# Kernel tuning notes

Measured on AMD Instinct MI355X. Metric: run time of the kernel, lower is better.

Reference implementation:

```python
import jax, jax.numpy as jnp
import numpy as np

B, N, V, H, Z = 2048, 32, 10, 256, 64


def setup_inputs() -> dict:
    key = jax.random.key(0)
    ks = jax.random.split(key, 14)
    # strictly upper-triangular random DAG adjacency (topological order = vertex index)
    p = jax.random.uniform(ks[0], (B, N, N))
    tri = jnp.triu(jnp.ones((N, N), jnp.float32), k=1)
    adj = (p < 0.12).astype(jnp.float32) * tri
    node_types = jax.random.randint(ks[1], (B, N), 0, V).astype(jnp.int32)
    s = 0.05
    return dict(
        adj=adj,
        node_types=node_types,
        w_ih=jax.random.normal(ks[2], (V, 3 * H), jnp.float32) * s,
        w_hh=jax.random.normal(ks[3], (H, 3 * H), jnp.float32) * s,
        b_ih=jax.random.normal(ks[4], (3 * H,), jnp.float32) * s,
        b_hh=jax.random.normal(ks[5], (3 * H,), jnp.float32) * s,
        w_gate=jax.random.normal(ks[6], (H, H), jnp.float32) * s,
        b_gate=jax.random.normal(ks[7], (H,), jnp.float32) * s,
        w_map=jax.random.normal(ks[8], (H, H), jnp.float32) * s,
        w_mu=jax.random.normal(ks[9], (H, Z), jnp.float32) * s,
        b_mu=jax.random.normal(ks[10], (Z,), jnp.float32) * s,
        w_std=jax.random.normal(ks[11], (H, Z), jnp.float32) * s,
        b_std=jax.random.normal(ks[12], (Z,), jnp.float32) * s,
    )


def _gru_cell(x, h, w_ih, w_hh, b_ih, b_hh):
    # torch GRUCell math; weights stored [in, 3H]
    gi = x @ w_ih + b_ih  # [B, 3H]
    gh = h @ w_hh + b_hh
    i_r, i_z, i_n = jnp.split(gi, 3, axis=-1)
    h_r, h_z, h_n = jnp.split(gh, 3, axis=-1)
    r = jax.nn.sigmoid(i_r + h_r)
    z = jax.nn.sigmoid(i_z + h_z)
    n = jnp.tanh(i_n + r * h_n)
    return (1.0 - z) * n + z * h


def reference(adj, node_types, w_ih, w_hh, b_ih, b_hh, w_gate, b_gate, w_map,
              w_mu, b_mu, w_std, b_std):
    x_all = jax.nn.one_hot(node_types, V, dtype=adj.dtype)  # [B, N, V]
    hidden0 = jnp.zeros((B, N, H), adj.dtype)
    adj_cols = jnp.transpose(adj, (2, 0, 1))  # [N, B, N]; col v = predecessor mask of v
    x_seq = jnp.transpose(x_all, (1, 0, 2))   # [N, B, V]

    def step(hidden, inps):
        col, x, v = inps
        # gate(h_pred) * map(h_pred), summed over predecessors. map has no bias,
        # so non-predecessor (zero-masked) rows contribute exactly zero, matching
        # the padded-gather formulation in the original code.
        gm = jax.nn.sigmoid(hidden @ w_gate + b_gate) * (hidden @ w_map)  # [B, N, H]
        agg = jnp.einsum('bn,bnh->bh', col, gm)  # [B, H]; zero for v=0 (no preds)
        h_new = _gru_cell(x, agg, w_ih, w_hh, b_ih, b_hh)  # [B, H]
        hidden = jax.lax.dynamic_update_slice(hidden, h_new[:, None, :], (0, v, 0))
        return hidden, None

    hidden, _ = jax.lax.scan(step, hidden0, (adj_cols, x_seq, jnp.arange(N)))
    hg = hidden[:, -1, :]  # graph state = last vertex hidden
    mu = hg @ w_mu + b_mu
    sigma = hg @ w_std + b_std
    return (mu, sigma)
```

## Files before the change

### kernel.cpp

```cpp
#include <hip/hip_runtime.h>


#define BB 2048
#define NN 32
#define VV 10
#define HH 256
#define ZZ 64
#define BT 8
#define KC 8
#define NT1 48
#define NT2 32
#define WHH_ELEMS (NT1 * KC * 64 * 8)
#define WGM_ELEMS (NT2 * KC * 64 * 8)
#define DYN_LDS_BYTES (BT * NN * HH * 2)

typedef __attribute__((ext_vector_type(8))) short frag8;
typedef __attribute__((ext_vector_type(4))) float facc4;

__device__ __forceinline__ float bf2f(unsigned short u) {
    unsigned int x = ((unsigned int)u) << 16;
    return __builtin_bit_cast(float, x);
}
__device__ __forceinline__ unsigned short f2bf(float f) {
    unsigned int x = __builtin_bit_cast(unsigned int, f);
    x += 0x7FFFu + ((x >> 16) & 1u);
    return (unsigned short)(x >> 16);
}
__device__ __forceinline__ float sigm(float x) { return 1.0f / (1.0f + __expf(-x)); }
__device__ __forceinline__ float ldv(const float* p, size_t i) { return p[i]; }
__device__ __forceinline__ float ldv(const unsigned short* p, size_t i) { return bf2f(p[i]); }
__device__ __forceinline__ void stv(float* p, size_t i, float v) { p[i] = v; }
__device__ __forceinline__ void stv(unsigned short* p, size_t i, float v) { p[i] = f2bf(v); }

__global__ void detect_dtype(const unsigned short* __restrict__ w, int* flag) {
    __shared__ int zc, bc;
    if (threadIdx.x == 0) { zc = 0; bc = 0; }
    __syncthreads();
    int z = 0, b = 0;
    for (int i = threadIdx.x; i < 2048; i += 256) {
        unsigned short lo = w[2 * i];
        if (lo == 0) z++;
        unsigned e = (lo >> 7) & 0xFFu;
        if (e >= 0x86u) b++;
    }
    atomicAdd(&zc, z); atomicAdd(&bc, b);
    __syncthreads();
    if (threadIdx.x == 0) *flag = (bc > 0 || zc > 512) ? 1 : 0;
}

template <typename T>
__global__ void repack_weights(const T* __restrict__ w_hh,
                               const T* __restrict__ w_gate,
                               const T* __restrict__ w_map,
                               unsigned short* __restrict__ whh_p,
                               unsigned short* __restrict__ wgm_p,
                               const int* __restrict__ flag, int want) {
    if (*flag != want) return;
    int t = blockIdx.x * blockDim.x + threadIdx.x;
    int lane = t & 63;
    int frag = t >> 6;
    int kbase = (lane >> 4) * 8;
    if (frag < NT1 * KC) {
        int jt = frag / KC, kc = frag % KC;
        int col = jt * 16 + (lane & 15);
        unsigned short* dst = whh_p + ((size_t)frag * 64 + lane) * 8;
        #pragma unroll
        for (int j = 0; j < 8; ++j)
            dst[j] = f2bf(ldv(w_hh, (size_t)(kc * 32 + kbase + j) * 768 + col));
    } else if (frag < (NT1 + NT2) * KC) {
        int f2 = frag - NT1 * KC;
        int jt = f2 / KC, kc = f2 % KC;
        int col = jt * 16 + (lane & 15);
        unsigned short* dst = wgm_p + ((size_t)f2 * 64 + lane) * 8;
        #pragma unroll
        for (int j = 0; j < 8; ++j) {
            int k = kc * 32 + kbase + j;
            dst[j] = f2bf((col < HH) ? ldv(w_gate, (size_t)k * HH + col)
                                     : ldv(w_map, (size_t)k * HH + (col - HH)));
        }
    }
}

template <typename T>
__global__ __launch_bounds__(1024, 4) void vae_main(
    const T* __restrict__ adj,
    const int* __restrict__ ntypes,
    const T* __restrict__ w_ih,
    const T* __restrict__ b_ih,
    const T* __restrict__ b_hh,
    const T* __restrict__ b_gate,
    const T* __restrict__ w_mu,
    const T* __restrict__ b_mu,
    const T* __restrict__ w_std,
    const T* __restrict__ b_std,
    const unsigned short* __restrict__ whh_p,
    const unsigned short* __restrict__ wgm_p,
    T* __restrict__ out,
    const int* __restrict__ flag, int want)
{
    if (*flag != want) return;

    extern __shared__ __align__(16) char dyn_lds[];
    unsigned short* gmS = (unsigned short*)dyn_lds;

    __shared__ __align__(16) float agg[BT][HH];
    __shared__ __align__(16) unsigned short aggbf[BT][264];
    __shared__ __align__(16) unsigned short hnew[BT][264];
    __shared__ unsigned int  amask[BT][NN];
    __shared__ int           ntva[BT][NN];
    __shared__ unsigned short bihL[768], bhhL[768], bgL[HH];

    const int tid  = threadIdx.x;
    const int lane = tid & 63;
    const int w    = tid >> 6;
    const int b0   = blockIdx.x * BT;

    const frag8* whh8 = (const frag8*)whh_p;
    const frag8* wgm8 = (const frag8*)wgm_p;

    if (tid < 256) {
        int bi = tid >> 5, vv = tid & 31;
        unsigned m = 0;
        for (int n = 0; n < NN; ++n)
            if (ldv(adj, ((size_t)(b0 + bi) * NN + n) * NN + vv) != 0.0f) m |= (1u << n);
        amask[bi][vv] = m;
    } else if (tid < 512) {
        int idx = tid - 256;
        int bi = idx >> 5, vv = idx & 31;
        ntva[bi][vv] = ntypes[(b0 + bi) * NN + vv];
    }
    for (int i = tid; i < 768; i += 1024) {
        bihL[i] = f2bf(ldv(b_ih, i));
        bhhL[i] = f2bf(ldv(b_hh, i));
    }
    if (tid < HH) bgL[tid] = f2bf(ldv(b_gate, tid));

    frag8 wR[KC], wG[KC];
    {
        const frag8* pR = whh8 + (size_t)w * (KC * 64) + lane;
        const frag8* pG = wgm8 + (size_t)w * (KC * 64) + lane;
        #pragma unroll
        for (int kc = 0; kc < KC; ++kc) { wR[kc] = pR[kc * 64]; wG[kc] = pG[kc * 64]; }
    }
    __syncthreads();

    const int arow  = lane & 15;
    const int acol0 = (lane >> 4) * 8;

    for (int v = 0; v < NN; ++v) {
        if (w < BT) {
            const int bi = w;
            const int h4 = lane * 4;
            const unsigned short* rb = gmS + (size_t)(bi * NN) * HH + h4;
            unsigned m = amask[bi][v];
            float a0 = 0.f, a1 = 0.f, a2 = 0.f, a3 = 0.f;
            float c0 = 0.f, c1 = 0.f, c2 = 0.f, c3 = 0.f;
            while (m) {
                int n0 = __builtin_ctz(m); m &= m - 1;
                const ushort4 g0 = *(const ushort4*)(rb + n0 * HH);
                if (m) {
                    int n1 = __builtin_ctz(m); m &= m - 1;
                    const ushort4 g1 = *(const ushort4*)(rb + n1 * HH);
                    c0 += bf2f(g1.x); c1 += bf2f(g1.y);
                    c2 += bf2f(g1.z); c3 += bf2f(g1.w);
                }
                a0 += bf2f(g0.x); a1 += bf2f(g0.y);
                a2 += bf2f(g0.z); a3 += bf2f(g0.w);
            }
            a0 += c0; a1 += c1; a2 += c2; a3 += c3;
            *(float4*)&agg[bi][h4] = make_float4(a0, a1, a2, a3);
            ushort4 ab; ab.x = f2bf(a0); ab.y = f2bf(a1); ab.z = f2bf(a2); ab.w = f2bf(a3);
            *(ushort4*)&aggbf[bi][h4] = ab;
        }
        __syncthreads();

        {
            frag8 afrag[KC];
            if (arow < BT) {
                #pragma unroll
                for (int kc = 0; kc < KC; ++kc)
                    afrag[kc] = *(const frag8*)&aggbf[arow][kc * 32 + acol0];
            } else {
                #pragma unroll
                for (int kc = 0; kc < KC; ++kc) afrag[kc] = frag8{};
            }

            const int t = w;
            facc4 aR = {0.f, 0.f, 0.f, 0.f};
            facc4 aZ = {0.f, 0.f, 0.f, 0.f};
            facc4 aN = {0.f, 0.f, 0.f, 0.f};
            const frag8* pZ = whh8 + (size_t)(t + 16) * (KC * 64) + lane;
            const frag8* pN = whh8 + (size_t)(t + 32) * (KC * 64) + lane;
            #pragma unroll
            for (int kc = 0; kc < KC; ++kc) {
                aR = __builtin_amdgcn_mfma_f32_16x16x32_bf16(afrag[kc], wR[kc], aR, 0, 0, 0);
                aZ = __builtin_amdgcn_mfma_f32_16x16x32_bf16(afrag[kc], pZ[kc * 64], aZ, 0, 0, 0);
                aN = __builtin_amdgcn_mfma_f32_16x16x32_bf16(afrag[kc], pN[kc * 64], aN, 0, 0, 0);
            }
            const int col = t * 16 + (lane & 15);
            const int q = lane >> 4;
            if (q < 2) {
                const float bir  = bf2f(bihL[col]),       bhr = bf2f(bhhL[col]);
                const float biz  = bf2f(bihL[col + 256]), bhz = bf2f(bhhL[col + 256]);
                const float bin_ = bf2f(bihL[col + 512]), bhn = bf2f(bhhL[col + 512]);
                #pragma unroll
                for (int i = 0; i < 4; ++i) {
                    const int bi = 4 * q + i;
                    const size_t ty = (size_t)ntva[bi][v] * 768;
                    const float xr = ldv(w_ih, ty + col);
                    const float xz = ldv(w_ih, ty + col + 256);
                    const float xn = ldv(w_ih, ty + col + 512);
                    const float r = sigm(xr + bir + aR[i] + bhr);
                    const float z = sigm(xz + biz + aZ[i] + bhz);
                    const float n = tanhf(xn + bin_ + r * (aN[i] + bhn));
                    const float h = (1.f - z) * n + z * agg[bi][col];
                    hnew[bi][col] = f2bf(h);
                }
            }
        }
        __syncthreads();

        {
            frag8 hfrag[KC];
            if (arow < BT) {
                #pragma unroll
                for (int kc = 0; kc < KC; ++kc)
                    hfrag[kc] = *(const frag8*)&hnew[arow][kc * 32 + acol0];
            } else {
                #pragma unroll
                for (int kc = 0; kc < KC; ++kc) hfrag[kc] = frag8{};
            }

            const int t = w;
            facc4 aG = {0.f, 0.f, 0.f, 0.f};
            facc4 aM = {0.f, 0.f, 0.f, 0.f};
            const frag8* pM = wgm8 + (size_t)(t + 16) * (KC * 64) + lane;
            #pragma unroll
            for (int kc = 0; kc < KC; ++kc) {
                aG = __builtin_amdgcn_mfma_f32_16x16x32_bf16(hfrag[kc], wG[kc], aG, 0, 0, 0);
                aM = __builtin_amdgcn_mfma_f32_16x16x32_bf16(hfrag[kc], pM[kc * 64], aM, 0, 0, 0);
            }
            const int col = t * 16 + (lane & 15);
            const int q = lane >> 4;
            if (q < 2) {
                const float bg = bf2f(bgL[col]);
                #pragma unroll
                for (int i = 0; i < 4; ++i) {
                    const int bi = 4 * q + i;
                    gmS[(size_t)(bi * NN + v) * HH + col] = f2bf(sigm(aG[i] + bg) * aM[i]);
                }
            }
        }
        __syncthreads();
    }

    {
        const int bi = w >> 1, half = w & 1, z = lane;
        float am = 0.f, as = 0.f;
        const int h0 = half * 128;
        #pragma unroll 4
        for (int h = h0; h < h0 + 128; ++h) {
            const float hv = bf2f(hnew[bi][h]);
            am += hv * ldv(w_mu, (size_t)h * ZZ + z);
            as += hv * ldv(w_std, (size_t)h * ZZ + z);
        }
        agg[bi][half * 64 + z]       = am;
        agg[bi][128 + half * 64 + z] = as;
    }
    __syncthreads();
    if (w < BT) {
        const int bi = w, z = lane;
        const float am = agg[bi][z] + agg[bi][64 + z] + ldv(b_mu, z);
        const float as = agg[bi][128 + z] + agg[bi][192 + z] + ldv(b_std, z);
        stv(out, (size_t)(b0 + bi) * ZZ + z, am);
        stv(out, (size_t)BB * ZZ + (size_t)(b0 + bi) * ZZ + z, as);
    }
}

extern "C" void kernel_launch(void* const* d_in, const int* in_sizes, int n_in,
                              void* d_out, int out_size, void* d_ws, size_t ws_size,
                              hipStream_t stream)
{
    unsigned short* whh_p = (unsigned short*)d_ws;
    unsigned short* wgm_p = whh_p + WHH_ELEMS;

    size_t flag_off = (ws_size >= 8) ? ((ws_size - 4) & ~(size_t)3) : 0;
    int* flag = (int*)((char*)d_ws + flag_off);

    (void)hipFuncSetAttribute(reinterpret_cast<const void*>(&vae_main<float>),
                              hipFuncAttributeMaxDynamicSharedMemorySize, DYN_LDS_BYTES);
    (void)hipFuncSetAttribute(reinterpret_cast<const void*>(&vae_main<unsigned short>),
                              hipFuncAttributeMaxDynamicSharedMemorySize, DYN_LDS_BYTES);

    detect_dtype<<<dim3(1), 256, 0, stream>>>((const unsigned short*)d_in[2], flag);

    repack_weights<float><<<dim3(160), 256, 0, stream>>>(
        (const float*)d_in[3], (const float*)d_in[6], (const float*)d_in[8],
        whh_p, wgm_p, flag, 1);
    repack_weights<unsigned short><<<dim3(160), 256, 0, stream>>>(
        (const unsigned short*)d_in[3], (const unsigned short*)d_in[6],
        (const unsigned short*)d_in[8], whh_p, wgm_p, flag, 0);

    vae_main<float><<<dim3(BB / BT), 1024, DYN_LDS_BYTES, stream>>>(
        (const float*)d_in[0], (const int*)d_in[1], (const float*)d_in[2],
        (const float*)d_in[4], (const float*)d_in[5], (const float*)d_in[7],
        (const float*)d_in[9], (const float*)d_in[10], (const float*)d_in[11],
        (const float*)d_in[12], whh_p, wgm_p, (float*)d_out, flag, 1);
    vae_main<unsigned short><<<dim3(BB / BT), 1024, DYN_LDS_BYTES, stream>>>(
        (const unsigned short*)d_in[0], (const int*)d_in[1],
        (const unsigned short*)d_in[2], (const unsigned short*)d_in[4],
        (const unsigned short*)d_in[5], (const unsigned short*)d_in[7],
        (const unsigned short*)d_in[9], (const unsigned short*)d_in[10],
        (const unsigned short*)d_in[11], (const unsigned short*)d_in[12],
        whh_p, wgm_p, (unsigned short*)d_out, flag, 0);
}
```

Baseline: 601.1 us.

## Halve workgroup to 512 threads with each wave computing two column tiles

Cuts the block from 16 to 8 waves, so each wave now handles two 16-column tiles of both the GRU and the gate/map matmuls. Weight fragments are reloaded from global memory each step instead of being kept in registers across the whole recurrence. Biases are kept in LDS as fp32, and the final mu/sigma projection is done by one wave per batch row, dropping a reduction and a barrier. This trades per-step weight reload traffic and lower thread-level parallelism for fewer waves contending at the barriers, and possibly more resident blocks per CU given LDS limits.

```diff
diff --git a/kernel.cpp b/kernel.cpp
--- a/kernel.cpp
+++ b/kernel.cpp
@@ -82,7 +82,7 @@
 }
 
 template <typename T>
-__global__ __launch_bounds__(1024, 4) void vae_main(
+__global__ __launch_bounds__(512, 2) void vae_main(
     const T* __restrict__ adj,
     const int* __restrict__ ntypes,
     const T* __restrict__ w_ih,
@@ -108,7 +108,7 @@
     __shared__ __align__(16) unsigned short hnew[BT][264];
     __shared__ unsigned int  amask[BT][NN];
     __shared__ int           ntva[BT][NN];
-    __shared__ unsigned short bihL[768], bhhL[768], bgL[HH];
+    __shared__ float bihL[768], bhhL[768], bgL[HH];
 
     const int tid  = threadIdx.x;
     const int lane = tid & 63;
@@ -124,31 +124,20 @@
         for (int n = 0; n < NN; ++n)
             if (ldv(adj, ((size_t)(b0 + bi) * NN + n) * NN + vv) != 0.0f) m |= (1u << n);
         amask[bi][vv] = m;
-    } else if (tid < 512) {
+    } else {
         int idx = tid - 256;
         int bi = idx >> 5, vv = idx & 31;
         ntva[bi][vv] = ntypes[(b0 + bi) * NN + vv];
     }
-    for (int i = tid; i < 768; i += 1024) {
-        bihL[i] = f2bf(ldv(b_ih, i));
-        bhhL[i] = f2bf(ldv(b_hh, i));
-    }
-    if (tid < HH) bgL[tid] = f2bf(ldv(b_gate, tid));
-
-    frag8 wR[KC], wG[KC];
-    {
-        const frag8* pR = whh8 + (size_t)w * (KC * 64) + lane;
-        const frag8* pG = wgm8 + (size_t)w * (KC * 64) + lane;
-        #pragma unroll
-        for (int kc = 0; kc < KC; ++kc) { wR[kc] = pR[kc * 64]; wG[kc] = pG[kc * 64]; }
-    }
+    for (int i = tid; i < 768; i += 512) { bihL[i] = ldv(b_ih, i); bhhL[i] = ldv(b_hh, i); }
+    if (tid < HH) bgL[tid] = ldv(b_gate, tid);
     __syncthreads();
 
     const int arow  = lane & 15;
     const int acol0 = (lane >> 4) * 8;
 
     for (int v = 0; v < NN; ++v) {
-        if (w < BT) {
+        {
             const int bi = w;
             const int h4 = lane * 4;
             const unsigned short* rb = gmS + (size_t)(bi * NN) * HH + h4;
@@ -185,36 +174,55 @@
                 for (int kc = 0; kc < KC; ++kc) afrag[kc] = frag8{};
             }
 
-            const int t = w;
-            facc4 aR = {0.f, 0.f, 0.f, 0.f};
-            facc4 aZ = {0.f, 0.f, 0.f, 0.f};
-            facc4 aN = {0.f, 0.f, 0.f, 0.f};
-            const frag8* pZ = whh8 + (size_t)(t + 16) * (KC * 64) + lane;
-            const frag8* pN = whh8 + (size_t)(t + 32) * (KC * 64) + lane;
+            frag8 R0[KC], Z0[KC], N0[KC], R1[KC], Z1[KC], N1[KC];
+            {
+                const frag8* pR0 = whh8 + (size_t)(w     ) * (KC * 64) + lane;
+                const frag8* pZ0 = whh8 + (size_t)(w + 16) * (KC * 64) + lane;
+                const frag8* pN0 = whh8 + (size_t)(w + 32) * (KC * 64) + lane;
+                const frag8* pR1 = whh8 + (size_t)(w +  8) * (KC * 64) + lane;
+                const frag8* pZ1 = whh8 + (size_t)(w + 24) * (KC * 64) + lane;
+                const frag8* pN1 = whh8 + (size_t)(w + 40) * (KC * 64) + lane;
+                #pragma unroll
+                for (int kc = 0; kc < KC; ++kc) {
+                    R0[kc] = pR0[kc * 64]; Z0[kc] = pZ0[kc * 64]; N0[kc] = pN0[kc * 64];
+                }
+                #pragma unroll
+                for (int kc = 0; kc < KC; ++kc) {
+                    R1[kc] = pR1[kc * 64]; Z1[kc] = pZ1[kc * 64]; N1[kc] = pN1[kc * 64];
+                }
+            }
+
             #pragma unroll
-            for (int kc = 0; kc < KC; ++kc) {
-                aR = __builtin_amdgcn_mfma_f32_16x16x32_bf16(afrag[kc], wR[kc], aR, 0, 0, 0);
-                aZ = __builtin_amdgcn_mfma_f32_16x16x32_bf16(afrag[kc], pZ[kc * 64], aZ, 0, 0, 0);
-                aN = __builtin_amdgcn_mfma_f32_16x16x32_bf16(afrag[kc], pN[kc * 64], aN, 0, 0, 0);
-            }
-            const int col = t * 16 + (lane & 15);
-            const int q = lane >> 4;
-            if (q < 2) {
-                const float bir  = bf2f(bihL[col]),       bhr = bf2f(bhhL[col]);
-                const float biz  = bf2f(bihL[col + 256]), bhz = bf2f(bhhL[col + 256]);
-                const float bin_ = bf2f(bihL[col + 512]), bhn = bf2f(bhhL[col + 512]);
-                #pragma unroll
-                for (int i = 0; i < 4; ++i) {
-                    const int bi = 4 * q + i;
-                    const size_t ty = (size_t)ntva[bi][v] * 768;
-                    const float xr = ldv(w_ih, ty + col);
-                    const float xz = ldv(w_ih, ty + col + 256);
-                    const float xn = ldv(w_ih, ty + col + 512);
-                    const float r = sigm(xr + bir + aR[i] + bhr);
-                    const float z = sigm(xz + biz + aZ[i] + bhz);
-                    const float n = tanhf(xn + bin_ + r * (aN[i] + bhn));
-                    const float h = (1.f - z) * n + z * agg[bi][col];
-                    hnew[bi][col] = f2bf(h);
+            for (int tt = 0; tt < 2; ++tt) {
+                const int t = w + tt * 8;
+                facc4 aR = {0.f, 0.f, 0.f, 0.f};
+                facc4 aZ = {0.f, 0.f, 0.f, 0.f};
+                facc4 aN = {0.f, 0.f, 0.f, 0.f};
+                #pragma unroll
+                for (int kc = 0; kc < KC; ++kc) {
+                    aR = __builtin_amdgcn_mfma_f32_16x16x32_bf16(afrag[kc], tt ? R1[kc] : R0[kc], aR, 0, 0, 0);
+                    aZ = __builtin_amdgcn_mfma_f32_16x16x32_bf16(afrag[kc], tt ? Z1[kc] : Z0[kc], aZ, 0, 0, 0);
+                    aN = __builtin_amdgcn_mfma_f32_16x16x32_bf16(afrag[kc], tt ? N1[kc] : N0[kc], aN, 0, 0, 0);
+                }
+                const int col = t * 16 + (lane & 15);
+                const int q = lane >> 4;
+                if (q < 2) {
+                    const float bir  = bihL[col],       bhr = bhhL[col];
+                    const float biz  = bihL[col + 256], bhz = bhhL[col + 256];
+                    const float bin_ = bihL[col + 512], bhn = bhhL[col + 512];
+                    #pragma unroll
+                    for (int i = 0; i < 4; ++i) {
+                        const int bi = 4 * q + i;
+                        const size_t ty = (size_t)ntva[bi][v] * 768;
+                        const float xr = ldv(w_ih, ty + col);
+                        const float xz = ldv(w_ih, ty + col + 256);
+                        const float xn = ldv(w_ih, ty + col + 512);
+                        const float r = sigm(xr + bir + aR[i] + bhr);
+                        const float z = sigm(xz + biz + aZ[i] + bhz);
+                        const float n = tanhf(xn + bin_ + r * (aN[i] + bhn));
+                        const float h = (1.f - z) * n + z * agg[bi][col];
+                        hnew[bi][col] = f2bf(h);
+                    }
                 }
             }
         }
@@ -231,23 +239,38 @@
                 for (int kc = 0; kc < KC; ++kc) hfrag[kc] = frag8{};
             }
 
-            const int t = w;
-            facc4 aG = {0.f, 0.f, 0.f, 0.f};
-            facc4 aM = {0.f, 0.f, 0.f, 0.f};
-            const frag8* pM = wgm8 + (size_t)(t + 16) * (KC * 64) + lane;
+            frag8 G0[KC], M0[KC], G1[KC], M1[KC];
+            {
+                const frag8* pG0 = wgm8 + (size_t)(w     ) * (KC * 64) + lane;
+                const frag8* pM0 = wgm8 + (size_t)(w + 16) * (KC * 64) + lane;
+                const frag8* pG1 = wgm8 + (size_t)(w +  8) * (KC * 64) + lane;
+                const frag8* pM1 = wgm8 + (size_t)(w + 24) * (KC * 64) + lane;
+                #pragma unroll
+                for (int kc = 0; kc < KC; ++kc) {
+                    G0[kc] = pG0[kc * 64]; M0[kc] = pM0[kc * 64];
+                    G1[kc] = pG1[kc * 64]; M1[kc] = pM1[kc * 64];
+                }
+            }
+
             #pragma unroll
-            for (int kc = 0; kc < KC; ++kc) {
-                aG = __builtin_amdgcn_mfma_f32_16x16x32_bf16(hfrag[kc], wG[kc], aG, 0, 0, 0);
-                aM = __builtin_amdgcn_mfma_f32_16x16x32_bf16(hfrag[kc], pM[kc * 64], aM, 0, 0, 0);
-            }
-            const int col = t * 16 + (lane & 15);
-            const int q = lane >> 4;
-            if (q < 2) {
-                const float bg = bf2f(bgL[col]);
-                #pragma unroll
-                for (int i = 0; i < 4; ++i) {
-                    const int bi = 4 * q + i;
-                    gmS[(size_t)(bi * NN + v) * HH + col] = f2bf(sigm(aG[i] + bg) * aM[i]);
+            for (int tt = 0; tt < 2; ++tt) {
+                const int t = w + tt * 8;
+                facc4 aG = {0.f, 0.f, 0.f, 0.f};
+                facc4 aM = {0.f, 0.f, 0.f, 0.f};
+                #pragma unroll
+                for (int kc = 0; kc < KC; ++kc) {
+                    aG = __builtin_amdgcn_mfma_f32_16x16x32_bf16(hfrag[kc], tt ? G1[kc] : G0[kc], aG, 0, 0, 0);
+                    aM = __builtin_amdgcn_mfma_f32_16x16x32_bf16(hfrag[kc], tt ? M1[kc] : M0[kc], aM, 0, 0, 0);
+                }
+                const int col = t * 16 + (lane & 15);
+                const int q = lane >> 4;
+                if (q < 2) {
+                    const float bg = bgL[col];
+                    #pragma unroll
+                    for (int i = 0; i < 4; ++i) {
+                        const int bi = 4 * q + i;
+                        gmS[(size_t)(bi * NN + v) * HH + col] = f2bf(sigm(aG[i] + bg) * aM[i]);
+                    }
                 }
             }
         }
@@ -255,23 +278,14 @@
     }
 
     {
-        const int bi = w >> 1, half = w & 1, z = lane;
-        float am = 0.f, as = 0.f;
-        const int h0 = half * 128;
-        #pragma unroll 4
-        for (int h = h0; h < h0 + 128; ++h) {
+        const int bi = w, z = lane;
+        float am = ldv(b_mu, z);
+        float as = ldv(b_std, z);
+        for (int h = 0; h < HH; ++h) {
             const float hv = bf2f(hnew[bi][h]);
             am += hv * ldv(w_mu, (size_t)h * ZZ + z);
             as += hv * ldv(w_std, (size_t)h * ZZ + z);
         }
-        agg[bi][half * 64 + z]       = am;
-        agg[bi][128 + half * 64 + z] = as;
-    }
-    __syncthreads();
-    if (w < BT) {
-        const int bi = w, z = lane;
-        const float am = agg[bi][z] + agg[bi][64 + z] + ldv(b_mu, z);
-        const float as = agg[bi][128 + z] + agg[bi][192 + z] + ldv(b_std, z);
         stv(out, (size_t)(b0 + bi) * ZZ + z, am);
         stv(out, (size_t)BB * ZZ + (size_t)(b0 + bi) * ZZ + z, as);
     }
@@ -301,12 +315,12 @@
         (const unsigned short*)d_in[3], (const unsigned short*)d_in[6],
         (const unsigned short*)d_in[8], whh_p, wgm_p, flag, 0);
 
-    vae_main<float><<<dim3(BB / BT), 1024, DYN_LDS_BYTES, stream>>>(
+    vae_main<float><<<dim3(BB / BT), 512, DYN_LDS_BYTES, stream>>>(
         (const float*)d_in[0], (const int*)d_in[1], (const float*)d_in[2],
         (const float*)d_in[4], (const float*)d_in[5], (const float*)d_in[7],
         (const float*)d_in[9], (const float*)d_in[10], (const float*)d_in[11],
         (const float*)d_in[12], whh_p, wgm_p, (float*)d_out, flag, 1);
-    vae_main<unsigned short><<<dim3(BB / BT), 1024, DYN_LDS_BYTES, stream>>>(
+    vae_main<unsigned short><<<dim3(BB / BT), 512, DYN_LDS_BYTES, stream>>>(
         (const unsigned short*)d_in[0], (const int*)d_in[1],
         (const unsigned short*)d_in[2], (const unsigned short*)d_in[4],
         (const unsigned short*)d_in[5], (const unsigned short*)d_in[7],
```

New measurement: 621.7 us. +3.4%, slower.

## Stage fused input weights in LDS, prefetch streamed MFMA weights, split aggregation across all waves

Applied to the files above, without the earlier changes.

The w_ih rows with b_ih folded in are staged into LDS as bf16, replacing per-step global loads of w_ih. The hidden-hidden and gate/map weight fragments are no longer held in registers; they are streamed from global memory with one-step-ahead software prefetch, which frees registers at the cost of more global or cache traffic. Predecessor aggregation now uses all 16 waves with 2 columns each, and the float agg buffer is dropped, so the GRU reads the previous hidden from the bf16 copy, which slightly lowers precision. The final mu/sigma projection is split by output instead of by half of H, removing one barrier.

```diff
diff --git a/kernel.cpp b/kernel.cpp
--- a/kernel.cpp
+++ b/kernel.cpp
@@ -103,12 +103,12 @@
     extern __shared__ __align__(16) char dyn_lds[];
     unsigned short* gmS = (unsigned short*)dyn_lds;
 
-    __shared__ __align__(16) float agg[BT][HH];
     __shared__ __align__(16) unsigned short aggbf[BT][264];
     __shared__ __align__(16) unsigned short hnew[BT][264];
+    __shared__ __align__(16) unsigned short wihL[VV * 776];
     __shared__ unsigned int  amask[BT][NN];
     __shared__ int           ntva[BT][NN];
-    __shared__ unsigned short bihL[768], bhhL[768], bgL[HH];
+    __shared__ float bhhL[768], bgL[HH];
 
     const int tid  = threadIdx.x;
     const int lane = tid & 63;
@@ -129,48 +129,37 @@
         int bi = idx >> 5, vv = idx & 31;
         ntva[bi][vv] = ntypes[(b0 + bi) * NN + vv];
     }
-    for (int i = tid; i < 768; i += 1024) {
-        bihL[i] = f2bf(ldv(b_ih, i));
-        bhhL[i] = f2bf(ldv(b_hh, i));
-    }
-    if (tid < HH) bgL[tid] = f2bf(ldv(b_gate, tid));
-
-    frag8 wR[KC], wG[KC];
-    {
-        const frag8* pR = whh8 + (size_t)w * (KC * 64) + lane;
-        const frag8* pG = wgm8 + (size_t)w * (KC * 64) + lane;
-        #pragma unroll
-        for (int kc = 0; kc < KC; ++kc) { wR[kc] = pR[kc * 64]; wG[kc] = pG[kc * 64]; }
-    }
+    for (int i = tid; i < VV * 768; i += 1024) {
+        int r = i / 768, c = i - r * 768;
+        wihL[r * 776 + c] = f2bf(ldv(w_ih, (size_t)i) + ldv(b_ih, (size_t)c));
+    }
+    for (int i = tid; i < 768; i += 1024) bhhL[i] = ldv(b_hh, i);
+    if (tid < HH) bgL[tid] = ldv(b_gate, tid);
     __syncthreads();
 
     const int arow  = lane & 15;
     const int acol0 = (lane >> 4) * 8;
 
     for (int v = 0; v < NN; ++v) {
-        if (w < BT) {
-            const int bi = w;
-            const int h4 = lane * 4;
-            const unsigned short* rb = gmS + (size_t)(bi * NN) * HH + h4;
+        {
+            const int bi = w >> 1;
+            const int c0 = (w & 1) * 128 + lane * 2;
+            const unsigned short* rb = gmS + (size_t)(bi * NN) * HH + c0;
             unsigned m = amask[bi][v];
-            float a0 = 0.f, a1 = 0.f, a2 = 0.f, a3 = 0.f;
-            float c0 = 0.f, c1 = 0.f, c2 = 0.f, c3 = 0.f;
+            float a0 = 0.f, a1 = 0.f, c0f = 0.f, c1f = 0.f;
             while (m) {
                 int n0 = __builtin_ctz(m); m &= m - 1;
-                const ushort4 g0 = *(const ushort4*)(rb + n0 * HH);
+                const ushort2 g0 = *(const ushort2*)(rb + n0 * HH);
                 if (m) {
                     int n1 = __builtin_ctz(m); m &= m - 1;
-                    const ushort4 g1 = *(const ushort4*)(rb + n1 * HH);
-                    c0 += bf2f(g1.x); c1 += bf2f(g1.y);
-                    c2 += bf2f(g1.z); c3 += bf2f(g1.w);
+                    const ushort2 g1 = *(const ushort2*)(rb + n1 * HH);
+                    c0f += bf2f(g1.x); c1f += bf2f(g1.y);
                 }
                 a0 += bf2f(g0.x); a1 += bf2f(g0.y);
-                a2 += bf2f(g0.z); a3 += bf2f(g0.w);
-            }
-            a0 += c0; a1 += c1; a2 += c2; a3 += c3;
-            *(float4*)&agg[bi][h4] = make_float4(a0, a1, a2, a3);
-            ushort4 ab; ab.x = f2bf(a0); ab.y = f2bf(a1); ab.z = f2bf(a2); ab.w = f2bf(a3);
-            *(ushort4*)&aggbf[bi][h4] = ab;
+            }
+            a0 += c0f; a1 += c1f;
+            ushort2 ab; ab.x = f2bf(a0); ab.y = f2bf(a1);
+            *(ushort2*)&aggbf[bi][c0] = ab;
         }
         __syncthreads();
 
@@ -186,35 +175,44 @@
             }
 
             const int t = w;
+            const frag8* pR = whh8 + (size_t)(t     ) * (KC * 64) + lane;
+            const frag8* pZ = whh8 + (size_t)(t + 16) * (KC * 64) + lane;
+            const frag8* pN = whh8 + (size_t)(t + 32) * (KC * 64) + lane;
+            frag8 bR = pR[0], bZ = pZ[0], bN = pN[0];
             facc4 aR = {0.f, 0.f, 0.f, 0.f};
             facc4 aZ = {0.f, 0.f, 0.f, 0.f};
             facc4 aN = {0.f, 0.f, 0.f, 0.f};
-            const frag8* pZ = whh8 + (size_t)(t + 16) * (KC * 64) + lane;
-            const frag8* pN = whh8 + (size_t)(t + 32) * (KC * 64) + lane;
             #pragma unroll
             for (int kc = 0; kc < KC; ++kc) {
-                aR = __builtin_amdgcn_mfma_f32_16x16x32_bf16(afrag[kc], wR[kc], aR, 0, 0, 0);
-                aZ = __builtin_amdgcn_mfma_f32_16x16x32_bf16(afrag[kc], pZ[kc * 64], aZ, 0, 0, 0);
-                aN = __builtin_amdgcn_mfma_f32_16x16x32_bf16(afrag[kc], pN[kc * 64], aN, 0, 0, 0);
+                frag8 nR{}, nZ{}, nN{};
+                if (kc + 1 < KC) {
+                    nR = pR[(kc + 1) * 64];
+                    nZ = pZ[(kc + 1) * 64];
+                    nN = pN[(kc + 1) * 64];
+                }
+                aR = __builtin_amdgcn_mfma_f32_16x16x32_bf16(afrag[kc], bR, aR, 0, 0, 0);
+                aZ = __builtin_amdgcn_mfma_f32_16x16x32_bf16(afrag[kc], bZ, aZ, 0, 0, 0);
+                aN = __builtin_amdgcn_mfma_f32_16x16x32_bf16(afrag[kc], bN, aN, 0, 0, 0);
+                bR = nR; bZ = nZ; bN = nN;
             }
             const int col = t * 16 + (lane & 15);
             const int q = lane >> 4;
             if (q < 2) {
-                const float bir  = bf2f(bihL[col]),       bhr = bf2f(bhhL[col]);
-                const float biz  = bf2f(bihL[col + 256]), bhz = bf2f(bhhL[col + 256]);
-                const float bin_ = bf2f(bihL[col + 512]), bhn = bf2f(bhhL[col + 512]);
+                const float bhr = bhhL[col];
+                const float bhz = bhhL[col + 256];
+                const float bhn = bhhL[col + 512];
                 #pragma unroll
                 for (int i = 0; i < 4; ++i) {
                     const int bi = 4 * q + i;
-                    const size_t ty = (size_t)ntva[bi][v] * 768;
-                    const float xr = ldv(w_ih, ty + col);
-                    const float xz = ldv(w_ih, ty + col + 256);
-                    const float xn = ldv(w_ih, ty + col + 512);
-                    const float r = sigm(xr + bir + aR[i] + bhr);
-                    const float z = sigm(xz + biz + aZ[i] + bhz);
-                    const float n = tanhf(xn + bin_ + r * (aN[i] + bhn));
-                    const float h = (1.f - z) * n + z * agg[bi][col];
-                    hnew[bi][col] = f2bf(h);
+                    const int ty = ntva[bi][v] * 776;
+                    const float xr = bf2f(wihL[ty + col]);
+                    const float xz = bf2f(wihL[ty + col + 256]);
+                    const float xn = bf2f(wihL[ty + col + 512]);
+                    const float r = sigm(xr + aR[i] + bhr);
+                    const float z = sigm(xz + aZ[i] + bhz);
+                    const float n = tanhf(xn + r * (aN[i] + bhn));
+                    const float hp = bf2f(aggbf[bi][col]);
+                    hnew[bi][col] = f2bf((1.f - z) * n + z * hp);
                 }
             }
         }
@@ -232,18 +230,26 @@
             }
 
             const int t = w;
+            const frag8* pG = wgm8 + (size_t)(t     ) * (KC * 64) + lane;
+            const frag8* pM = wgm8 + (size_t)(t + 16) * (KC * 64) + lane;
+            frag8 bG = pG[0], bM = pM[0];
             facc4 aG = {0.f, 0.f, 0.f, 0.f};
             facc4 aM = {0.f, 0.f, 0.f, 0.f};
-            const frag8* pM = wgm8 + (size_t)(t + 16) * (KC * 64) + lane;
             #pragma unroll
             for (int kc = 0; kc < KC; ++kc) {
-                aG = __builtin_amdgcn_mfma_f32_16x16x32_bf16(hfrag[kc], wG[kc], aG, 0, 0, 0);
-                aM = __builtin_amdgcn_mfma_f32_16x16x32_bf16(hfrag[kc], pM[kc * 64], aM, 0, 0, 0);
+                frag8 nG{}, nM{};
+                if (kc + 1 < KC) {
+                    nG = pG[(kc + 1) * 64];
+                    nM = pM[(kc + 1) * 64];
+                }
+                aG = __builtin_amdgcn_mfma_f32_16x16x32_bf16(hfrag[kc], bG, aG, 0, 0, 0);
+                aM = __builtin_amdgcn_mfma_f32_16x16x32_bf16(hfrag[kc], bM, aM, 0, 0, 0);
+                bG = nG; bM = nM;
             }
             const int col = t * 16 + (lane & 15);
             const int q = lane >> 4;
             if (q < 2) {
-                const float bg = bf2f(bgL[col]);
+                const float bg = bgL[col];
                 #pragma unroll
                 for (int i = 0; i < 4; ++i) {
                     const int bi = 4 * q + i;
@@ -255,25 +261,17 @@
     }
 
     {
-        const int bi = w >> 1, half = w & 1, z = lane;
-        float am = 0.f, as = 0.f;
-        const int h0 = half * 128;
+        const int bi = w & 7, z = lane;
+        const bool is_mu = (w < 8);
+        float acc = is_mu ? ldv(b_mu, z) : ldv(b_std, z);
+        const T* wm = is_mu ? w_mu : w_std;
         #pragma unroll 4
-        for (int h = h0; h < h0 + 128; ++h) {
+        for (int h = 0; h < HH; ++h) {
             const float hv = bf2f(hnew[bi][h]);
-            am += hv * ldv(w_mu, (size_t)h * ZZ + z);
-            as += hv * ldv(w_std, (size_t)h * ZZ + z);
-        }
-        agg[bi][half * 64 + z]       = am;
-        agg[bi][128 + half * 64 + z] = as;
-    }
-    __syncthreads();
-    if (w < BT) {
-        const int bi = w, z = lane;
-        const float am = agg[bi][z] + agg[bi][64 + z] + ldv(b_mu, z);
-        const float as = agg[bi][128 + z] + agg[bi][192 + z] + ldv(b_std, z);
-        stv(out, (size_t)(b0 + bi) * ZZ + z, am);
-        stv(out, (size_t)BB * ZZ + (size_t)(b0 + bi) * ZZ + z, as);
+            acc += hv * ldv(wm, (size_t)h * ZZ + z);
+        }
+        const size_t off = is_mu ? 0 : (size_t)BB * ZZ;
+        stv(out, off + (size_t)(b0 + bi) * ZZ + z, acc);
     }
 }
 
```

Result: no change. 603.4 us (+0.4%).

## Double batch tile to fill MFMA rows, spill half of gm state to global workspace

Applied to the files above, without the earlier changes.

Raises the per-block batch tile from 8 to 16 so every row of each 16x16 MFMA carries a real graph instead of zero padding, which halves the number of blocks. The gate*map state for the extra 8 graphs lives in a per-block global workspace slab because LDS only holds 8 graphs' worth. Weights are now streamed from global or cache in every step instead of being kept in registers, and the biases are stored in LDS as fp32. The main kernel is launched in chunks sized to the available workspace. The cost is extra global-memory traffic and latency on the serial 32-step recurrence.

```diff
diff --git a/kernel.cpp b/kernel.cpp
--- a/kernel.cpp
+++ b/kernel.cpp
@@ -6,13 +6,17 @@
 #define VV 10
 #define HH 256
 #define ZZ 64
-#define BT 8
+#define BT 16
 #define KC 8
 #define NT1 48
 #define NT2 32
 #define WHH_ELEMS (NT1 * KC * 64 * 8)
 #define WGM_ELEMS (NT2 * KC * 64 * 8)
-#define DYN_LDS_BYTES (BT * NN * HH * 2)
+#define GM_BYTE_OFF ((WHH_ELEMS + WGM_ELEMS) * 2)
+#define SLAB_ELEMS (8 * NN * HH)
+#define SLAB_BYTES (SLAB_ELEMS * 2)
+#define DYN_LDS_BYTES (8 * NN * HH * 2)
+#define NBLK (BB / BT)
 
 typedef __attribute__((ext_vector_type(8))) short frag8;
 typedef __attribute__((ext_vector_type(4))) float facc4;
@@ -95,7 +99,9 @@
     const T* __restrict__ b_std,
     const unsigned short* __restrict__ whh_p,
     const unsigned short* __restrict__ wgm_p,
+    unsigned short* __restrict__ gm_base,
     T* __restrict__ out,
+    int b_start,
     const int* __restrict__ flag, int want)
 {
     if (*flag != want) return;
@@ -103,72 +109,77 @@
     extern __shared__ __align__(16) char dyn_lds[];
     unsigned short* gmS = (unsigned short*)dyn_lds;
 
-    __shared__ __align__(16) float agg[BT][HH];
     __shared__ __align__(16) unsigned short aggbf[BT][264];
     __shared__ __align__(16) unsigned short hnew[BT][264];
     __shared__ unsigned int  amask[BT][NN];
     __shared__ int           ntva[BT][NN];
-    __shared__ unsigned short bihL[768], bhhL[768], bgL[HH];
+    __shared__ float bihL[768], bhhL[768], bgL[HH];
 
     const int tid  = threadIdx.x;
     const int lane = tid & 63;
     const int w    = tid >> 6;
-    const int b0   = blockIdx.x * BT;
+    const int b0   = b_start + blockIdx.x * BT;
+
+    unsigned short* gmG = gm_base + (size_t)blockIdx.x * SLAB_ELEMS;
 
     const frag8* whh8 = (const frag8*)whh_p;
     const frag8* wgm8 = (const frag8*)wgm_p;
 
-    if (tid < 256) {
+    if (tid < 512) {
         int bi = tid >> 5, vv = tid & 31;
         unsigned m = 0;
         for (int n = 0; n < NN; ++n)
             if (ldv(adj, ((size_t)(b0 + bi) * NN + n) * NN + vv) != 0.0f) m |= (1u << n);
         amask[bi][vv] = m;
-    } else if (tid < 512) {
-        int idx = tid - 256;
+    } else {
+        int idx = tid - 512;
         int bi = idx >> 5, vv = idx & 31;
         ntva[bi][vv] = ntypes[(b0 + bi) * NN + vv];
     }
-    for (int i = tid; i < 768; i += 1024) {
-        bihL[i] = f2bf(ldv(b_ih, i));
-        bhhL[i] = f2bf(ldv(b_hh, i));
-    }
-    if (tid < HH) bgL[tid] = f2bf(ldv(b_gate, tid));
-
-    frag8 wR[KC], wG[KC];
-    {
-        const frag8* pR = whh8 + (size_t)w * (KC * 64) + lane;
-        const frag8* pG = wgm8 + (size_t)w * (KC * 64) + lane;
-        #pragma unroll
-        for (int kc = 0; kc < KC; ++kc) { wR[kc] = pR[kc * 64]; wG[kc] = pG[kc * 64]; }
-    }
+    for (int i = tid; i < 768; i += 1024) { bihL[i] = ldv(b_ih, i); bhhL[i] = ldv(b_hh, i); }
+    if (tid < HH) bgL[tid] = ldv(b_gate, tid);
     __syncthreads();
 
     const int arow  = lane & 15;
     const int acol0 = (lane >> 4) * 8;
 
     for (int v = 0; v < NN; ++v) {
-        if (w < BT) {
+        {
             const int bi = w;
             const int h4 = lane * 4;
-            const unsigned short* rb = gmS + (size_t)(bi * NN) * HH + h4;
             unsigned m = amask[bi][v];
             float a0 = 0.f, a1 = 0.f, a2 = 0.f, a3 = 0.f;
             float c0 = 0.f, c1 = 0.f, c2 = 0.f, c3 = 0.f;
-            while (m) {
-                int n0 = __builtin_ctz(m); m &= m - 1;
-                const ushort4 g0 = *(const ushort4*)(rb + n0 * HH);
-                if (m) {
-                    int n1 = __builtin_ctz(m); m &= m - 1;
-                    const ushort4 g1 = *(const ushort4*)(rb + n1 * HH);
-                    c0 += bf2f(g1.x); c1 += bf2f(g1.y);
-                    c2 += bf2f(g1.z); c3 += bf2f(g1.w);
+            if (bi < 8) {
+                const unsigned short* rb = gmS + (size_t)(bi * NN) * HH + h4;
+                while (m) {
+                    int n0 = __builtin_ctz(m); m &= m - 1;
+                    const ushort4 g0 = *(const ushort4*)(rb + n0 * HH);
+                    if (m) {
+                        int n1 = __builtin_ctz(m); m &= m - 1;
+                        const ushort4 g1 = *(const ushort4*)(rb + n1 * HH);
+                        c0 += bf2f(g1.x); c1 += bf2f(g1.y);
+                        c2 += bf2f(g1.z); c3 += bf2f(g1.w);
+                    }
+                    a0 += bf2f(g0.x); a1 += bf2f(g0.y);
+                    a2 += bf2f(g0.z); a3 += bf2f(g0.w);
                 }
-                a0 += bf2f(g0.x); a1 += bf2f(g0.y);
-                a2 += bf2f(g0.z); a3 += bf2f(g0.w);
+            } else {
+                const unsigned short* rb = gmG + (size_t)((bi - 8) * NN) * HH + h4;
+                while (m) {
+                    int n0 = __builtin_ctz(m); m &= m - 1;
+                    const ushort4 g0 = *(const ushort4*)(rb + n0 * HH);
+                    if (m) {
+                        int n1 = __builtin_ctz(m); m &= m - 1;
+                        const ushort4 g1 = *(const ushort4*)(rb + n1 * HH);
+                        c0 += bf2f(g1.x); c1 += bf2f(g1.y);
+                        c2 += bf2f(g1.z); c3 += bf2f(g1.w);
+                    }
+                    a0 += bf2f(g0.x); a1 += bf2f(g0.y);
+                    a2 += bf2f(g0.z); a3 += bf2f(g0.w);
+                }
             }
             a0 += c0; a1 += c1; a2 += c2; a3 += c3;
-            *(float4*)&agg[bi][h4] = make_float4(a0, a1, a2, a3);
             ushort4 ab; ab.x = f2bf(a0); ab.y = f2bf(a1); ab.z = f2bf(a2); ab.w = f2bf(a3);
             *(ushort4*)&aggbf[bi][h4] = ab;
         }
@@ -176,102 +187,84 @@
 
         {
             frag8 afrag[KC];
-            if (arow < BT) {
-                #pragma unroll
-                for (int kc = 0; kc < KC; ++kc)
-                    afrag[kc] = *(const frag8*)&aggbf[arow][kc * 32 + acol0];
-            } else {
-                #pragma unroll
-                for (int kc = 0; kc < KC; ++kc) afrag[kc] = frag8{};
-            }
+            #pragma unroll
+            for (int kc = 0; kc < KC; ++kc)
+                afrag[kc] = *(const frag8*)&aggbf[arow][kc * 32 + acol0];
 
             const int t = w;
+            const frag8* pR = whh8 + (size_t)(t     ) * (KC * 64) + lane;
+            const frag8* pZ = whh8 + (size_t)(t + 16) * (KC * 64) + lane;
+            const frag8* pN = whh8 + (size_t)(t + 32) * (KC * 64) + lane;
             facc4 aR = {0.f, 0.f, 0.f, 0.f};
             facc4 aZ = {0.f, 0.f, 0.f, 0.f};
             facc4 aN = {0.f, 0.f, 0.f, 0.f};
-            const frag8* pZ = whh8 + (size_t)(t + 16) * (KC * 64) + lane;
-            const frag8* pN = whh8 + (size_t)(t + 32) * (KC * 64) + lane;
             #pragma unroll
             for (int kc = 0; kc < KC; ++kc) {
-                aR = __builtin_amdgcn_mfma_f32_16x16x32_bf16(afrag[kc], wR[kc], aR, 0, 0, 0);
+                aR = __builtin_amdgcn_mfma_f32_16x16x32_bf16(afrag[kc], pR[kc * 64], aR, 0, 0, 0);
                 aZ = __builtin_amdgcn_mfma_f32_16x16x32_bf16(afrag[kc], pZ[kc * 64], aZ, 0, 0, 0);
                 aN = __builtin_amdgcn_mfma_f32_16x16x32_bf16(afrag[kc], pN[kc * 64], aN, 0, 0, 0);
             }
             const int col = t * 16 + (lane & 15);
             const int q = lane >> 4;
-            if (q < 2) {
-                const float bir  = bf2f(bihL[col]),       bhr = bf2f(bhhL[col]);
-                const float biz  = bf2f(bihL[col + 256]), bhz = bf2f(bhhL[col + 256]);
-                const float bin_ = bf2f(bihL[col + 512]), bhn = bf2f(bhhL[col + 512]);
-                #pragma unroll
-                for (int i = 0; i < 4; ++i) {
-                    const int bi = 4 * q + i;
-                    const size_t ty = (size_t)ntva[bi][v] * 768;
-                    const float xr = ldv(w_ih, ty + col);
-                    const float xz = ldv(w_ih, ty + col + 256);
-                    const float xn = ldv(w_ih, ty + col + 512);
-                    const float r = sigm(xr + bir + aR[i] + bhr);
-                    const float z = sigm(xz + biz + aZ[i] + bhz);
-                    const float n = tanhf(xn + bin_ + r * (aN[i] + bhn));
-                    const float h = (1.f - z) * n + z * agg[bi][col];
-                    hnew[bi][col] = f2bf(h);
-                }
+            const float bir  = bihL[col],       bhr = bhhL[col];
+            const float biz  = bihL[col + 256], bhz = bhhL[col + 256];
+            const float bin_ = bihL[col + 512], bhn = bhhL[col + 512];
+            #pragma unroll
+            for (int i = 0; i < 4; ++i) {
+                const int bi = 4 * q + i;
+                const size_t ty = (size_t)ntva[bi][v] * 768;
+                const float xr = ldv(w_ih, ty + col);
+                const float xz = ldv(w_ih, ty + col + 256);
+                const float xn = ldv(w_ih, ty + col + 512);
+                const float r = sigm(xr + bir + aR[i] + bhr);
+                const float z = sigm(xz + biz + aZ[i] + bhz);
+                const float n = tanhf(xn + bin_ + r * (aN[i] + bhn));
+                const float hp = bf2f(aggbf[bi][col]);
+                hnew[bi][col] = f2bf((1.f - z) * n + z * hp);
             }
         }
         __syncthreads();
 
         {
             frag8 hfrag[KC];
-            if (arow < BT) {
-                #pragma unroll
-                for (int kc = 0; kc < KC; ++kc)
-                    hfrag[kc] = *(const frag8*)&hnew[arow][kc * 32 + acol0];
-            } else {
-                #pragma unroll
-                for (int kc = 0; kc < KC; ++kc) hfrag[kc] = frag8{};
-            }
+            #pragma unroll
+            for (int kc = 0; kc < KC; ++kc)
+                hfrag[kc] = *(const frag8*)&hnew[arow][kc * 32 + acol0];
 
             const int t = w;
+            const frag8* pG = wgm8 + (size_t)(t     ) * (KC * 64) + lane;
+            const frag8* pM = wgm8 + (size_t)(t + 16) * (KC * 64) + lane;
             facc4 aG = {0.f, 0.f, 0.f, 0.f};
             facc4 aM = {0.f, 0.f, 0.f, 0.f};
-            const frag8* pM = wgm8 + (size_t)(t + 16) * (KC * 64) + lane;
             #pragma unroll
             for (int kc = 0; kc < KC; ++kc) {
-                aG = __builtin_amdgcn_mfma_f32_16x16x32_bf16(hfrag[kc], wG[kc], aG, 0, 0, 0);
+                aG = __builtin_amdgcn_mfma_f32_16x16x32_bf16(hfrag[kc], pG[kc * 64], aG, 0, 0, 0);
                 aM = __builtin_amdgcn_mfma_f32_16x16x32_bf16(hfrag[kc], pM[kc * 64], aM, 0, 0, 0);
             }
             const int col = t * 16 + (lane & 15);
             const int q = lane >> 4;
-            if (q < 2) {
-                const float bg = bf2f(bgL[col]);
-                #pragma unroll
-                for (int i = 0; i < 4; ++i) {
-                    const int bi = 4 * q + i;
-                    gmS[(size_t)(bi * NN + v) * HH + col] = f2bf(sigm(aG[i] + bg) * aM[i]);
-                }
+            const float bg = bgL[col];
+            #pragma unroll
+            for (int i = 0; i < 4; ++i) {
+                const int bi = 4 * q + i;
+                const unsigned short gv = f2bf(sigm(aG[i] + bg) * aM[i]);
+                if (bi < 8) gmS[(size_t)(bi * NN + v) * HH + col] = gv;
+                else        gmG[(size_t)((bi - 8) * NN + v) * HH + col] = gv;
             }
         }
         __syncthreads();
     }
 
     {
-        const int bi = w >> 1, half = w & 1, z = lane;
-        float am = 0.f, as = 0.f;
-        const int h0 = half * 128;
+        const int bi = w, z = lane;
+        float am = ldv(b_mu, z);
+        float as = ldv(b_std, z);
         #pragma unroll 4
-        for (int h = h0; h < h0 + 128; ++h) {
+        for (int h = 0; h < HH; ++h) {
             const float hv = bf2f(hnew[bi][h]);
             am += hv * ldv(w_mu, (size_t)h * ZZ + z);
             as += hv * ldv(w_std, (size_t)h * ZZ + z);
         }
-        agg[bi][half * 64 + z]       = am;
-        agg[bi][128 + half * 64 + z] = as;
-    }
-    __syncthreads();
-    if (w < BT) {
-        const int bi = w, z = lane;
-        const float am = agg[bi][z] + agg[bi][64 + z] + ldv(b_mu, z);
-        const float as = agg[bi][128 + z] + agg[bi][192 + z] + ldv(b_std, z);
         stv(out, (size_t)(b0 + bi) * ZZ + z, am);
         stv(out, (size_t)BB * ZZ + (size_t)(b0 + bi) * ZZ + z, as);
     }
@@ -283,9 +276,15 @@
 {
     unsigned short* whh_p = (unsigned short*)d_ws;
     unsigned short* wgm_p = whh_p + WHH_ELEMS;
+    unsigned short* gm_base = wgm_p + WGM_ELEMS;
 
     size_t flag_off = (ws_size >= 8) ? ((ws_size - 4) & ~(size_t)3) : 0;
     int* flag = (int*)((char*)d_ws + flag_off);
+
+    long long avail = (long long)flag_off - (long long)GM_BYTE_OFF;
+    int cb = (int)(avail / SLAB_BYTES);
+    if (cb < 1) cb = 1;
+    if (cb > NBLK) cb = NBLK;
 
     (void)hipFuncSetAttribute(reinterpret_cast<const void*>(&vae_main<float>),
                               hipFuncAttributeMaxDynamicSharedMemorySize, DYN_LDS_BYTES);
@@ -301,16 +300,20 @@
         (const unsigned short*)d_in[3], (const unsigned short*)d_in[6],
         (const unsigned short*)d_in[8], whh_p, wgm_p, flag, 0);
 
-    vae_main<float><<<dim3(BB / BT), 1024, DYN_LDS_BYTES, stream>>>(
-        (const float*)d_in[0], (const int*)d_in[1], (const float*)d_in[2],
-        (const float*)d_in[4], (const float*)d_in[5], (const float*)d_in[7],
-        (const float*)d_in[9], (const float*)d_in[10], (const float*)d_in[11],
-        (const float*)d_in[12], whh_p, wgm_p, (float*)d_out, flag, 1);
-    vae_main<unsigned short><<<dim3(BB / BT), 1024, DYN_LDS_BYTES, stream>>>(
-        (const unsigned short*)d_in[0], (const int*)d_in[1],
-        (const unsigned short*)d_in[2], (const unsigned short*)d_in[4],
-        (const unsigned short*)d_in[5], (const unsigned short*)d_in[7],
-        (const unsigned short*)d_in[9], (const unsigned short*)d_in[10],
-        (const unsigned short*)d_in[11], (const unsigned short*)d_in[12],
-        whh_p, wgm_p, (unsigned short*)d_out, flag, 0);
-}
+    for (int blk0 = 0; blk0 < NBLK; blk0 += cb) {
+        int g = NBLK - blk0; if (g > cb) g = cb;
+        vae_main<float><<<dim3(g), 1024, DYN_LDS_BYTES, stream>>>(
+            (const float*)d_in[0], (const int*)d_in[1], (const float*)d_in[2],
+            (const float*)d_in[4], (const float*)d_in[5], (const float*)d_in[7],
+            (const float*)d_in[9], (const float*)d_in[10], (const float*)d_in[11],
+            (const float*)d_in[12],
+            whh_p, wgm_p, gm_base, (float*)d_out, blk0 * BT, flag, 1);
+        vae_main<unsigned short><<<dim3(g), 1024, DYN_LDS_BYTES, stream>>>(
+            (const unsigned short*)d_in[0], (const int*)d_in[1],
+            (const unsigned short*)d_in[2], (const unsigned short*)d_in[4],
+            (const unsigned short*)d_in[5], (const unsigned short*)d_in[7],
+            (const unsigned short*)d_in[9], (const unsigned short*)d_in[10],
+            (const unsigned short*)d_in[11], (const unsigned short*)d_in[12],
+            whh_p, wgm_p, gm_base, (unsigned short*)d_out, blk0 * BT, flag, 0);
+    }
+}
```

New measurement: 630.9 us. 1.05x slower.
